# Kernel optimization log

Hardware: AMD Instinct MI355X
Metric: run time of the kernel (lower is better)

## Reference

```python
import jax, jax.numpy as jnp
import numpy as np

# Each of the 16 soft logic gates g(a,b) is affine in {1, a, b, a*b}.
# COEFF[g] = [k0, ka, kb, kab] so that gate_g = k0 + ka*a + kb*b + kab*a*b.
COEFF = np.array([
    [0,  0,  0,  0],   # 0: False
    [0,  0,  0,  1],   # 1: a AND b
    [0,  1,  0, -1],   # 2: a AND NOT b
    [0,  1,  0,  0],   # 3: a
    [0,  0,  1, -1],   # 4: NOT a AND b
    [0,  0,  1,  0],   # 5: b
    [0,  1,  1, -2],   # 6: XOR
    [0,  1,  1, -1],   # 7: OR
    [1, -1, -1,  1],   # 8: NOR
    [1, -1, -1,  2],   # 9: XNOR
    [1,  0, -1,  0],   # 10: NOT b
    [1,  0, -1,  1],   # 11: a OR NOT b
    [1, -1,  0,  0],   # 12: NOT a
    [1, -1,  0,  1],   # 13: NOT a OR b
    [1,  0,  0, -1],   # 14: NAND
    [1,  0,  0,  0],   # 15: True
], dtype=np.float32)

BATCH, IN_DIM, OUT_DIM, N_GATES = 2048, 16384, 16384, 16


def setup_inputs() -> dict:
    key = jax.random.key(0)
    k1, k2, k3, k4 = jax.random.split(key, 4)
    x = jax.random.uniform(k1, (BATCH, IN_DIM), dtype=jnp.float32)
    weights = jax.random.normal(k2, (OUT_DIM, N_GATES), dtype=jnp.float32)
    idx_a = jax.random.randint(k3, (OUT_DIM,), 0, IN_DIM, dtype=jnp.int64)
    idx_b = jax.random.randint(k4, (OUT_DIM,), 0, IN_DIM, dtype=jnp.int64)
    return {"x": x, "weights": weights, "idx_a": idx_a, "idx_b": idx_b}


def reference(x, weights, idx_a, idx_b):
    # Training-mode forward: softmax mixture over the 16 logic gates.
    nw = jax.nn.softmax(weights, axis=-1)            # [out, 16]
    W = nw @ jnp.asarray(COEFF, dtype=x.dtype)       # [out, 4] effective affine coeffs
    a = x[:, idx_a]                                  # [batch, out]
    b = x[:, idx_b]                                  # [batch, out]
    ab = a * b
    # r = sum_g nw[:,g] * gate_g(a,b) == W0 + Wa*a + Wb*b + Wab*ab
    return W[:, 0] + W[:, 1] * a + W[:, 2] * b + W[:, 3] * ab
```

## Files before the change

kernel.cpp:

```cpp
#include <hip/hip_runtime.h>

#define BATCH   2048
#define IN_DIM  16384
#define OUT_DIM 16384
#define NGATES  16

typedef float f32x4 __attribute__((ext_vector_type(4)));

__constant__ float c_coeff[NGATES][4] = {
    {0, 0, 0, 0},  {0, 0, 0, 1},  {0, 1, 0, -1}, {0, 1, 0, 0},
    {0, 0, 1, -1}, {0, 0, 1, 0},  {0, 1, 1, -2}, {0, 1, 1, -1},
    {1, -1, -1, 1},{1, -1, -1, 2},{1, 0, -1, 0}, {1, 0, -1, 1},
    {1, -1, 0, 0}, {1, -1, 0, 1}, {1, 0, 0, -1}, {1, 0, 0, 0}
};

__global__ __launch_bounds__(256) void prep_kernel(
    const float* __restrict__ weights,
    const int*   __restrict__ idx_a,
    const int*   __restrict__ idx_b,
    float4*      __restrict__ Wp,
    unsigned*    __restrict__ Ipk)
{
    int j = blockIdx.x * blockDim.x + threadIdx.x;
    if (j >= OUT_DIM) return;

    const float4* wrow = reinterpret_cast<const float4*>(weights + (size_t)j * NGATES);
    float v[NGATES];
    float4 q0 = wrow[0], q1 = wrow[1], q2 = wrow[2], q3 = wrow[3];
    v[0]=q0.x; v[1]=q0.y; v[2]=q0.z; v[3]=q0.w;
    v[4]=q1.x; v[5]=q1.y; v[6]=q1.z; v[7]=q1.w;
    v[8]=q2.x; v[9]=q2.y; v[10]=q2.z; v[11]=q2.w;
    v[12]=q3.x; v[13]=q3.y; v[14]=q3.z; v[15]=q3.w;

    float m = v[0];
#pragma unroll
    for (int g = 1; g < NGATES; ++g) m = fmaxf(m, v[g]);
    float s = 0.f;
#pragma unroll
    for (int g = 0; g < NGATES; ++g) { v[g] = expf(v[g] - m); s += v[g]; }
    float inv = 1.0f / s;

    float c0 = 0.f, c1 = 0.f, c2 = 0.f, c3 = 0.f;
#pragma unroll
    for (int g = 0; g < NGATES; ++g) {
        c0 += v[g] * c_coeff[g][0];
        c1 += v[g] * c_coeff[g][1];
        c2 += v[g] * c_coeff[g][2];
        c3 += v[g] * c_coeff[g][3];
    }
    Wp[j] = make_float4(c0 * inv, c1 * inv, c2 * inv, c3 * inv);
    Ipk[j] = (unsigned)idx_a[j] | ((unsigned)idx_b[j] << 16);
}

__global__ __launch_bounds__(1024) void logic_row_kernel(
    const float*  __restrict__ x,
    const float4* __restrict__ Wp,
    const uint4*  __restrict__ Ipk4,
    float*        __restrict__ out)
{
    __shared__ float row[IN_DIM];

    const int i = blockIdx.x;
    const float4* xr = reinterpret_cast<const float4*>(x + (size_t)i * IN_DIM);
    float4* rr = reinterpret_cast<float4*>(row);
#pragma unroll
    for (int k = 0; k < IN_DIM / 4 / 1024; ++k)
        rr[threadIdx.x + k * 1024] = xr[threadIdx.x + k * 1024];
    __syncthreads();

    f32x4* o4 = reinterpret_cast<f32x4*>(out + (size_t)i * OUT_DIM);

#pragma unroll
    for (int k = 0; k < OUT_DIM / 4 / 1024; ++k) {
        const int j4 = threadIdx.x + k * 1024;
        const int j = j4 * 4;
        float4 w0 = Wp[j], w1 = Wp[j + 1], w2 = Wp[j + 2], w3 = Wp[j + 3];
        uint4 ii = Ipk4[j4];

        float a0 = row[ii.x & 0xFFFFu], b0 = row[ii.x >> 16];
        float a1 = row[ii.y & 0xFFFFu], b1 = row[ii.y >> 16];
        float a2 = row[ii.z & 0xFFFFu], b2 = row[ii.z >> 16];
        float a3 = row[ii.w & 0xFFFFu], b3 = row[ii.w >> 16];

        f32x4 r;
        r.x = w0.x + w0.y * a0 + w0.z * b0 + w0.w * (a0 * b0);
        r.y = w1.x + w1.y * a1 + w1.z * b1 + w1.w * (a1 * b1);
        r.z = w2.x + w2.y * a2 + w2.z * b2 + w2.w * (a2 * b2);
        r.w = w3.x + w3.y * a3 + w3.z * b3 + w3.w * (a3 * b3);
        __builtin_nontemporal_store(r, &o4[j4]);
    }
}

extern "C" void kernel_launch(void* const* d_in, const int* in_sizes, int n_in,
                              void* d_out, int out_size, void* d_ws, size_t ws_size,
                              hipStream_t stream) {
    const float* x       = (const float*)d_in[0];
    const float* weights = (const float*)d_in[1];
    const int*   idx_a   = (const int*)d_in[2];
    const int*   idx_b   = (const int*)d_in[3];
    float* out = (float*)d_out;

    float4*   Wp  = (float4*)d_ws;
    unsigned* Ipk = (unsigned*)((char*)d_ws + (size_t)OUT_DIM * sizeof(float4));

    prep_kernel<<<(OUT_DIM + 255) / 256, 256, 0, stream>>>(weights, idx_a, idx_b, Wp, Ipk);
    logic_row_kernel<<<BATCH, 1024, 0, stream>>>(x, Wp, (const uint4*)Ipk, out);
}
```

Baseline: 59.40 us.

## Process eight rows per block with double-buffered async LDS staging

Each block now handles eight batch rows instead of one. The per-output weights and packed indices are loaded into registers once per block and reused across all eight rows, which cuts repeated L2 reads of that table. The next x row is prefetched into a second LDS buffer with global_load_lds while the current row is gathered and stored, synchronized by a manual vmcnt wait and a barrier. This doubles LDS use to 128KB, limiting each CU to one block, and the hand-written vmcnt(4) count relies on assumptions about the order in which memory operations complete.

After: 110.2 us. 1.85x slower.

```diff
diff --git a/kernel.cpp b/kernel.cpp
--- a/kernel.cpp
+++ b/kernel.cpp
@@ -4,6 +4,8 @@
 #define IN_DIM  16384
 #define OUT_DIM 16384
 #define NGATES  16
+#define ROWS_PER_BLOCK 8
+#define NBLK (BATCH / ROWS_PER_BLOCK)
 
 typedef float f32x4 __attribute__((ext_vector_type(4)));
 
@@ -52,42 +54,70 @@
     Ipk[j] = (unsigned)idx_a[j] | ((unsigned)idx_b[j] << 16);
 }
 
-__global__ __launch_bounds__(1024) void logic_row_kernel(
+__device__ __forceinline__ void stage_row(const float* __restrict__ xrow,
+                                          float* lbuf, int tid)
+{
+#pragma unroll
+    for (int kk = 0; kk < 4; ++kk) {
+        __builtin_amdgcn_global_load_lds(
+            (const __attribute__((address_space(1))) void*)(xrow + tid * 4 + kk * 4096),
+            (__attribute__((address_space(3))) void*)(lbuf + tid * 4 + kk * 4096),
+            16, 0, 0);
+    }
+}
+
+__global__ __launch_bounds__(1024, 4) void logic_row_kernel(
     const float*  __restrict__ x,
     const float4* __restrict__ Wp,
     const uint4*  __restrict__ Ipk4,
     float*        __restrict__ out)
 {
-    __shared__ float row[IN_DIM];
+    __shared__ float buf[2][IN_DIM];
+    const int tid  = threadIdx.x;
+    const int row0 = blockIdx.x * ROWS_PER_BLOCK;
 
-    const int i = blockIdx.x;
-    const float4* xr = reinterpret_cast<const float4*>(x + (size_t)i * IN_DIM);
-    float4* rr = reinterpret_cast<float4*>(row);
+    uint4  ii[4];
+    float4 w[4][4];
 #pragma unroll
-    for (int k = 0; k < IN_DIM / 4 / 1024; ++k)
-        rr[threadIdx.x + k * 1024] = xr[threadIdx.x + k * 1024];
+    for (int k = 0; k < 4; ++k) {
+        ii[k] = Ipk4[tid + k * 1024];
+#pragma unroll
+        for (int q = 0; q < 4; ++q)
+            w[k][q] = Wp[(tid + k * 1024) * 4 + q];
+    }
+
+    stage_row(x + (size_t)row0 * IN_DIM, buf[0], tid);
     __syncthreads();
 
-    f32x4* o4 = reinterpret_cast<f32x4*>(out + (size_t)i * OUT_DIM);
+    for (int r = 0; r < ROWS_PER_BLOCK; ++r) {
+        if (r + 1 < ROWS_PER_BLOCK) {
+            stage_row(x + (size_t)(row0 + r + 1) * IN_DIM, buf[(r + 1) & 1], tid);
+            __builtin_amdgcn_sched_barrier(0);
+        }
+
+        const float* __restrict__ rowbuf = buf[r & 1];
+        f32x4* o4 = reinterpret_cast<f32x4*>(out + (size_t)(row0 + r) * OUT_DIM);
 
 #pragma unroll
-    for (int k = 0; k < OUT_DIM / 4 / 1024; ++k) {
-        const int j4 = threadIdx.x + k * 1024;
-        const int j = j4 * 4;
-        float4 w0 = Wp[j], w1 = Wp[j + 1], w2 = Wp[j + 2], w3 = Wp[j + 3];
-        uint4 ii = Ipk4[j4];
+        for (int k = 0; k < 4; ++k) {
+            uint4 q = ii[k];
+            float a0 = rowbuf[q.x & 0xFFFFu], b0 = rowbuf[q.x >> 16];
+            float a1 = rowbuf[q.y & 0xFFFFu], b1 = rowbuf[q.y >> 16];
+            float a2 = rowbuf[q.z & 0xFFFFu], b2 = rowbuf[q.z >> 16];
+            float a3 = rowbuf[q.w & 0xFFFFu], b3 = rowbuf[q.w >> 16];
 
-        float a0 = row[ii.x & 0xFFFFu], b0 = row[ii.x >> 16];
-        float a1 = row[ii.y & 0xFFFFu], b1 = row[ii.y >> 16];
-        float a2 = row[ii.z & 0xFFFFu], b2 = row[ii.z >> 16];
-        float a3 = row[ii.w & 0xFFFFu], b3 = row[ii.w >> 16];
+            f32x4 res;
+            res.x = w[k][0].x + w[k][0].y * a0 + w[k][0].z * b0 + w[k][0].w * (a0 * b0);
+            res.y = w[k][1].x + w[k][1].y * a1 + w[k][1].z * b1 + w[k][1].w * (a1 * b1);
+            res.z = w[k][2].x + w[k][2].y * a2 + w[k][2].z * b2 + w[k][2].w * (a2 * b2);
+            res.w = w[k][3].x + w[k][3].y * a3 + w[k][3].z * b3 + w[k][3].w * (a3 * b3);
+            __builtin_nontemporal_store(res, &o4[tid + k * 1024]);
+        }
 
-        f32x4 r;
-        r.x = w0.x + w0.y * a0 + w0.z * b0 + w0.w * (a0 * b0);
-        r.y = w1.x + w1.y * a1 + w1.z * b1 + w1.w * (a1 * b1);
-        r.z = w2.x + w2.y * a2 + w2.z * b2 + w2.w * (a2 * b2);
-        r.w = w3.x + w3.y * a3 + w3.z * b3 + w3.w * (a3 * b3);
-        __builtin_nontemporal_store(r, &o4[j4]);
+        if (r + 1 < ROWS_PER_BLOCK) {
+            asm volatile("s_waitcnt vmcnt(4)" ::: "memory");
+            __builtin_amdgcn_s_barrier();
+        }
     }
 }
 
@@ -104,5 +134,5 @@
     unsigned* Ipk = (unsigned*)((char*)d_ws + (size_t)OUT_DIM * sizeof(float4));
 
     prep_kernel<<<(OUT_DIM + 255) / 256, 256, 0, stream>>>(weights, idx_a, idx_b, Wp, Ipk);
-    logic_row_kernel<<<BATCH, 1024, 0, stream>>>(x, Wp, (const uint4*)Ipk, out);
+    logic_row_kernel<<<NBLK, 1024, 0, stream>>>(x, Wp, (const uint4*)Ipk, out);
 }
```
